# Kernel optimization log

Hardware: AMD Instinct MI355X
Metric: run time of the kernel (lower is better)

The kernel has to match this reference:

```python
import jax, jax.numpy as jnp
import numpy as np

H = 2048
V = 32000
B = 4            # 2 chosen + 2 rejected sequences
T = 1024
BETA = 0.1
IGNORE_INDEX = -100


def setup_inputs() -> dict:
    key = jax.random.key(0)
    k1, k2, k3, k4, k5 = jax.random.split(key, 5)
    x = jax.random.normal(k1, (B, T, H), dtype=jnp.float32)
    ref_x = jax.random.normal(k2, (B, T, H), dtype=jnp.float32)
    y = jax.random.randint(k3, (B, T), 0, V, dtype=jnp.int64)
    # Linear weights scaled ~1/sqrt(H) so logits are well-conditioned
    W = jax.random.normal(k4, (V, H), dtype=jnp.float32) * (1.0 / np.sqrt(H))
    W_ref = jax.random.normal(k5, (V, H), dtype=jnp.float32) * (1.0 / np.sqrt(H))
    return {"x": x, "ref_x": ref_x, "y": y, "W": W, "W_ref": W_ref}


def _avg_seq_logps(h, W, y, mask):
    # h: [B,T,H], W: [V,H] -> average per-sequence log-prob of the target tokens
    logits = jnp.einsum("bth,vh->btv", h, W)                 # [B,T,V]
    logps = jax.nn.log_softmax(logits, axis=-1)
    y_safe = jnp.where(mask, y, 0)
    per_tok = jnp.take_along_axis(logps, y_safe[..., None], axis=-1)[..., 0]  # [B,T]
    m = mask.astype(logps.dtype)
    return (per_tok * m).sum(-1) / m.sum(-1)                  # [B]


def reference(x, ref_x, y, W, W_ref):
    mask = y != IGNORE_INDEX
    logps = _avg_seq_logps(x, W, y, mask)
    # reference model path is computed without gradients (torch.no_grad in Liger)
    ref_logps = jax.lax.stop_gradient(_avg_seq_logps(ref_x, W_ref, y, mask))
    half = B // 2
    chosen, rejected = logps[:half], logps[half:]
    ref_chosen, ref_rejected = ref_logps[:half], ref_logps[half:]
    logits_diff = BETA * ((chosen - ref_chosen) - (rejected - ref_rejected))
    loss = -jax.nn.log_sigmoid(logits_diff).sum() / half
    return loss
```

## Files before the change

kernel.cpp:

```cpp
#include <hip/hip_runtime.h>
#include <cstdint>
#include <cstddef>

#define HDIM 2048
#define VOCAB 32000
#define BT 4096
#define NVB 125
#define BETA_F 0.1f
#define SCALE_X 16.0f
#define SCALE_W 64.0f
#define INV_SC (1.0f / (SCALE_X * SCALE_W))
#define ID_SCALE 0x7f7f7f7f

typedef float f32x16 __attribute__((ext_vector_type(16)));
typedef int i32x4v __attribute__((ext_vector_type(4)));
typedef int i32x8v __attribute__((ext_vector_type(8)));

__device__ __forceinline__ void async_lds16(const void* g, void* l) {
  __builtin_amdgcn_global_load_lds(
      (__attribute__((address_space(1))) void*)g,
      (__attribute__((address_space(3))) void*)l,
      16, 0, 0);
}

#define BAR() __builtin_amdgcn_s_barrier()
#define LGKM0() do { asm volatile("s_waitcnt lgkmcnt(0)" ::: "memory"); \
                     __builtin_amdgcn_sched_barrier(0); } while (0)
#define VMCNT(n) do { asm volatile("s_waitcnt vmcnt(" #n ")" ::: "memory"); \
                      __builtin_amdgcn_sched_barrier(0); } while (0)

__global__ void cast_fp8_kernel(const float* __restrict__ src,
                                uint4* __restrict__ dst, int n16, float scale) {
  int i = blockIdx.x * blockDim.x + threadIdx.x;
  int stride = gridDim.x * blockDim.x;
  for (; i < n16; i += stride) {
    const float4* s = (const float4*)src + (size_t)i * 4;
    uint4 o;
    {
      float4 a = s[0];
      int r = __builtin_amdgcn_cvt_pk_fp8_f32(a.x * scale, a.y * scale, 0, false);
      o.x = __builtin_amdgcn_cvt_pk_fp8_f32(a.z * scale, a.w * scale, r, true);
    }
    {
      float4 a = s[1];
      int r = __builtin_amdgcn_cvt_pk_fp8_f32(a.x * scale, a.y * scale, 0, false);
      o.y = __builtin_amdgcn_cvt_pk_fp8_f32(a.z * scale, a.w * scale, r, true);
    }
    {
      float4 a = s[2];
      int r = __builtin_amdgcn_cvt_pk_fp8_f32(a.x * scale, a.y * scale, 0, false);
      o.z = __builtin_amdgcn_cvt_pk_fp8_f32(a.z * scale, a.w * scale, r, true);
    }
    {
      float4 a = s[3];
      int r = __builtin_amdgcn_cvt_pk_fp8_f32(a.x * scale, a.y * scale, 0, false);
      o.w = __builtin_amdgcn_cvt_pk_fp8_f32(a.z * scale, a.w * scale, r, true);
    }
    dst[i] = o;
  }
}

__global__ __launch_bounds__(512, 2) void gemm_lse256(
    const unsigned char* __restrict__ Xq,
    const unsigned char* __restrict__ Xrq,
    const unsigned char* __restrict__ Wq,
    const unsigned char* __restrict__ Wrq,
    float2* __restrict__ part) {
  __shared__ __align__(16) char lds[2][2][2][8192];

  const int tid = threadIdx.x;
  const int lane = tid & 63;
  const int w = tid >> 6;
  const int wm = w >> 2;
  const int wn = w & 3;
  const int which = blockIdx.y;

  const int lin = blockIdx.x;
  const int nl = (lin & 7) * 250 + (lin >> 3);
  const int mb = nl & 15;
  const int nb = nl >> 4;

  const unsigned char* A = which ? Xrq : Xq;
  const unsigned char* B = which ? Wrq : Wq;
  float2* pp = part + (size_t)which * BT * NVB;

  const int lp = lane ^ (((lane >> 5) & 1) << 1);
  const int srow = (w >> 1) * 32 + (lp & 1) * 16 + ((lp >> 2) & 15);
  const int scol = ((lp >> 1) & 1) * 32 + (w & 1) * 16;
  const unsigned char* Ag = A + (size_t)(mb * 256 + srow) * HDIM + scol;
  const unsigned char* Bg = B + (size_t)(nb * 256 + srow) * HDIM + scol;

#define STAGE(opsel, buf, h, T) do {                                          \
    const unsigned char* _g = (opsel) ? Bg : Ag;                              \
    async_lds16(_g + (size_t)(h) * 128 * HDIM + (T) * 64,                     \
                &lds[buf][opsel][h][0] + w * 1024);                           \
  } while (0)

  const int l31 = lane & 31;
  const int khalf = (lane >> 5) * 32;
#define FRAG32(dst, halfptr, row) do {                                        \
    int _r = (row);                                                           \
    int _p = ((((_r >> 5) << 11) + ((_r & 15) << 6) + khalf +                 \
               (((_r >> 4) & 1) << 4)) ^ (((_r >> 3) & 1) << 5));             \
    i32x4v _lo = *(const i32x4v*)((halfptr) + _p);                            \
    i32x4v _hi = *(const i32x4v*)((halfptr) + _p + 1024);                     \
    dst = (i32x8v){_lo[0], _lo[1], _lo[2], _lo[3],                            \
                   _hi[0], _hi[1], _hi[2], _hi[3]};                           \
  } while (0)

  const char* Ah[2] = { &lds[0][0][wm][0], &lds[1][0][wm][0] };
  const char* Bh[2] = { &lds[0][1][wn >> 1][0], &lds[1][1][wn >> 1][0] };
  const int brow = (wn & 1) * 64;

  f32x16 acc[4][2] = {};
  i32x8v aF0, aF1, bF0, bF1;

#define READ_B(buf) do {                                                      \
    FRAG32(bF0, Bh[buf], brow + l31);                                         \
    FRAG32(bF1, Bh[buf], brow + 32 + l31);                                    \
  } while (0)
#define READ_A2(buf, mi0) do {                                                \
    FRAG32(aF0, Ah[buf], (mi0) * 32 + l31);                                   \
    FRAG32(aF1, Ah[buf], (mi0) * 32 + 32 + l31);                              \
  } while (0)
#define MFMA4(MI0) do {                                                       \
    __builtin_amdgcn_s_setprio(1);                                            \
    acc[MI0][0] = __builtin_amdgcn_mfma_scale_f32_32x32x64_f8f6f4(            \
        aF0, bF0, acc[MI0][0], 0, 0, 0, ID_SCALE, 0, ID_SCALE);               \
    acc[MI0][1] = __builtin_amdgcn_mfma_scale_f32_32x32x64_f8f6f4(            \
        aF0, bF1, acc[MI0][1], 0, 0, 0, ID_SCALE, 0, ID_SCALE);               \
    acc[(MI0) + 1][0] = __builtin_amdgcn_mfma_scale_f32_32x32x64_f8f6f4(      \
        aF1, bF0, acc[(MI0) + 1][0], 0, 0, 0, ID_SCALE, 0, ID_SCALE);         \
    acc[(MI0) + 1][1] = __builtin_amdgcn_mfma_scale_f32_32x32x64_f8f6f4(      \
        aF1, bF1, acc[(MI0) + 1][1], 0, 0, 0, ID_SCALE, 0, ID_SCALE);         \
    __builtin_amdgcn_s_setprio(0);                                            \
  } while (0)

  STAGE(0, 0, 0, 0); STAGE(0, 0, 1, 0); STAGE(1, 0, 0, 0); STAGE(1, 0, 1, 0);
  STAGE(1, 1, 0, 1); STAGE(1, 1, 1, 1);
  VMCNT(2);
  BAR();

  for (int i = 0; i < 16; ++i) {
    const int t1 = 2 * i + 1;
    const int se = (2 * i + 2 > 30) ? 30 : 2 * i + 2;
    const int so = (2 * i + 3 > 31) ? 31 : 2 * i + 3;

    READ_A2(0, 0); READ_B(0);
    STAGE(0, 1, 0, t1); STAGE(0, 1, 1, t1);
    BAR(); LGKM0();
    MFMA4(0);
    BAR();

    READ_A2(0, 2);
    STAGE(1, 0, 0, se); STAGE(1, 0, 1, se);
    VMCNT(2);
    BAR(); LGKM0();
    MFMA4(2);
    BAR();

    READ_A2(1, 0); READ_B(1);
    STAGE(0, 0, 0, se); STAGE(0, 0, 1, se);
    BAR(); LGKM0();
    MFMA4(0);
    BAR();

    READ_A2(1, 2);
    STAGE(1, 1, 0, so); STAGE(1, 1, 1, so);
    VMCNT(2);
    BAR(); LGKM0();
    MFMA4(2);
    BAR();
  }
  VMCNT(0);
  BAR();

  float* red = (float*)&lds[0][0][0][0];
#pragma unroll
  for (int mi = 0; mi < 4; ++mi) {
#pragma unroll
    for (int r = 0; r < 16; ++r) {
      float v0 = acc[mi][0][r] * INV_SC;
      float v1 = acc[mi][1][r] * INV_SC;
      float m = fmaxf(v0, v1);
#pragma unroll
      for (int o = 1; o < 32; o <<= 1) m = fmaxf(m, __shfl_xor(m, o, 64));
      float s = __expf(v0 - m) + __expf(v1 - m);
#pragma unroll
      for (int o = 1; o < 32; o <<= 1) s += __shfl_xor(s, o, 64);
      if (l31 == 0) {
        int row = wm * 128 + mi * 32 + (r & 3) + 8 * (r >> 2) + 4 * (lane >> 5);
        red[wn * 256 + row] = m;
        red[1024 + wn * 256 + row] = s;
      }
    }
  }
  __syncthreads();
  if (tid < 256) {
    float m0 = red[tid], m1 = red[256 + tid], m2 = red[512 + tid], m3 = red[768 + tid];
    float M = fmaxf(fmaxf(m0, m1), fmaxf(m2, m3));
    float S = red[1024 + tid] * __expf(m0 - M) + red[1280 + tid] * __expf(m1 - M) +
              red[1536 + tid] * __expf(m2 - M) + red[1792 + tid] * __expf(m3 - M);
    pp[(size_t)(mb * 256 + tid) * NVB + nb] = make_float2(M, S);
  }
#undef STAGE
#undef FRAG32
#undef READ_B
#undef READ_A2
#undef MFMA4
}

__global__ void target_logit(const float* __restrict__ x, const float* __restrict__ xr,
                             const float* __restrict__ W, const float* __restrict__ Wr,
                             const int* __restrict__ y, float* __restrict__ tlog) {
  int wid = (blockIdx.x * blockDim.x + threadIdx.x) >> 6;
  int lane = threadIdx.x & 63;
  int which = wid >> 12;
  int tok = wid & 4095;
  int yy = y[tok];
  int ys = (yy == -100) ? 0 : yy;
  const float* xv = (which ? xr : x) + (size_t)tok * HDIM;
  const float* wv = (which ? Wr : W) + (size_t)ys * HDIM;
  const float4* x4 = (const float4*)xv;
  const float4* w4 = (const float4*)wv;
  float sum = 0.f;
  for (int i = lane; i < HDIM / 4; i += 64) {
    float4 a = x4[i], b = w4[i];
    sum += a.x * b.x + a.y * b.y + a.z * b.z + a.w * b.w;
  }
#pragma unroll
  for (int o = 1; o < 64; o <<= 1) sum += __shfl_xor(sum, o, 64);
  if (lane == 0) tlog[wid] = sum;
}

__global__ void lse_combine(const float2* __restrict__ part,
                            const float* __restrict__ tlog,
                            float* __restrict__ ptok) {
  int wid = (blockIdx.x * blockDim.x + threadIdx.x) >> 6;
  int lane = threadIdx.x & 63;
  const float2* p = part + (size_t)wid * NVB;
  float m = -INFINITY, s = 0.f;
  for (int i = lane; i < NVB; i += 64) {
    float2 v = p[i];
    float M = fmaxf(m, v.x);
    s = s * __expf(m - M) + v.y * __expf(v.x - M);
    m = M;
  }
#pragma unroll
  for (int o = 1; o < 64; o <<= 1) {
    float mo = __shfl_xor(m, o, 64);
    float so = __shfl_xor(s, o, 64);
    float M = fmaxf(m, mo);
    s = s * __expf(m - M) + so * __expf(mo - M);
    m = M;
  }
  if (lane == 0) ptok[wid] = tlog[wid] - (m + logf(s));
}

__global__ void final_loss(const float* __restrict__ ptok,
                           const int* __restrict__ y, float* __restrict__ out) {
  __shared__ float rs[256];
  __shared__ float rc[256];
  __shared__ float seq[8];
  int tid = threadIdx.x;
  for (int s = 0; s < 8; ++s) {
    int which = s >> 2, b = s & 3;
    float lsum = 0.f, lcnt = 0.f;
    for (int t = tid; t < 1024; t += 256) {
      int yy = y[b * 1024 + t];
      if (yy != -100) {
        lsum += ptok[which * 4096 + b * 1024 + t];
        lcnt += 1.f;
      }
    }
    rs[tid] = lsum; rc[tid] = lcnt;
    __syncthreads();
    for (int o = 128; o > 0; o >>= 1) {
      if (tid < o) { rs[tid] += rs[tid + o]; rc[tid] += rc[tid + o]; }
      __syncthreads();
    }
    if (tid == 0) seq[s] = rs[0] / rc[0];
    __syncthreads();
  }
  if (tid == 0) {
    float d0 = BETA_F * ((seq[0] - seq[4]) - (seq[2] - seq[6]));
    float d1 = BETA_F * ((seq[1] - seq[5]) - (seq[3] - seq[7]));
    auto sp = [](float a) { return fmaxf(a, 0.f) + log1pf(expf(-fabsf(a))); };
    out[0] = (sp(-d0) + sp(-d1)) * 0.5f;
  }
}

extern "C" void kernel_launch(void* const* d_in, const int* in_sizes, int n_in,
                              void* d_out, int out_size, void* d_ws, size_t ws_size,
                              hipStream_t stream) {
  const float* x   = (const float*)d_in[0];
  const float* xr  = (const float*)d_in[1];
  const int*   y   = (const int*)d_in[2];
  const float* Wf  = (const float*)d_in[3];
  const float* Wrf = (const float*)d_in[4];
  float* out = (float*)d_out;

  char* ws = (char*)d_ws;
  size_t off = 0;
  auto alloc = [&](size_t bytes) -> void* {
    void* p = ws + off;
    off = (off + bytes + 255) & ~(size_t)255;
    return p;
  };
  unsigned char* Xq  = (unsigned char*)alloc((size_t)BT * HDIM);
  unsigned char* Xrq = (unsigned char*)alloc((size_t)BT * HDIM);
  unsigned char* Wq  = (unsigned char*)alloc((size_t)VOCAB * HDIM);
  unsigned char* Wrq = (unsigned char*)alloc((size_t)VOCAB * HDIM);
  float2* part = (float2*)alloc((size_t)2 * BT * NVB * sizeof(float2));
  float*  tlog = (float*)alloc((size_t)2 * BT * sizeof(float));
  float*  ptok = (float*)alloc((size_t)2 * BT * sizeof(float));

  cast_fp8_kernel<<<2048, 256, 0, stream>>>(x,  (uint4*)Xq,  BT * HDIM / 16, SCALE_X);
  cast_fp8_kernel<<<2048, 256, 0, stream>>>(xr, (uint4*)Xrq, BT * HDIM / 16, SCALE_X);
  cast_fp8_kernel<<<2048, 256, 0, stream>>>(Wf,  (uint4*)Wq,  VOCAB * HDIM / 16, SCALE_W);
  cast_fp8_kernel<<<2048, 256, 0, stream>>>(Wrf, (uint4*)Wrq, VOCAB * HDIM / 16, SCALE_W);

  dim3 gg(2000, 2);
  gemm_lse256<<<gg, 512, 0, stream>>>(Xq, Xrq, Wq, Wrq, part);

  target_logit<<<2048, 256, 0, stream>>>(x, xr, Wf, Wrf, y, tlog);
  lse_combine<<<2048, 256, 0, stream>>>(part, tlog, ptok);
  final_loss<<<1, 256, 0, stream>>>(ptok, y, out);
}
```

Before: 1.033 ms.

## Use 1024-thread blocks with per-wave 64x64 tiles and interleaved LDS/MFMA schedule

Doubles the GEMM workgroup from 8 to 16 waves, so each wave now owns a 64x64 output tile (four accumulators) instead of 128x64. The main loop is rewritten to interleave individual fragment reads with single MFMAs, prefetching the next stage's fragments before the last MFMA of each K step. It also drops explicit lgkmcnt waits in favor of sched barriers. The aim is better latency hiding and simpler staging (one A and one B async load per thread per stage), at the cost of more LDS traffic per MFMA and one block per CU instead of two.

```diff
diff --git a/kernel.cpp b/kernel.cpp
--- a/kernel.cpp
+++ b/kernel.cpp
@@ -24,8 +24,7 @@
 }
 
 #define BAR() __builtin_amdgcn_s_barrier()
-#define LGKM0() do { asm volatile("s_waitcnt lgkmcnt(0)" ::: "memory"); \
-                     __builtin_amdgcn_sched_barrier(0); } while (0)
+#define SCHED0() __builtin_amdgcn_sched_barrier(0)
 #define VMCNT(n) do { asm volatile("s_waitcnt vmcnt(" #n ")" ::: "memory"); \
                       __builtin_amdgcn_sched_barrier(0); } while (0)
 
@@ -60,7 +59,7 @@
   }
 }
 
-__global__ __launch_bounds__(512, 2) void gemm_lse256(
+__global__ __launch_bounds__(1024) void gemm_lse256(
     const unsigned char* __restrict__ Xq,
     const unsigned char* __restrict__ Xrq,
     const unsigned char* __restrict__ Wq,
@@ -84,16 +83,16 @@
   const unsigned char* B = which ? Wrq : Wq;
   float2* pp = part + (size_t)which * BT * NVB;
 
+  const int wp = w & 7;
   const int lp = lane ^ (((lane >> 5) & 1) << 1);
-  const int srow = (w >> 1) * 32 + (lp & 1) * 16 + ((lp >> 2) & 15);
-  const int scol = ((lp >> 1) & 1) * 32 + (w & 1) * 16;
+  const int srow = (w >> 3) * 128 + (wp >> 1) * 32 + (lp & 1) * 16 + ((lp >> 2) & 15);
+  const int scol = ((lp >> 1) & 1) * 32 + (wp & 1) * 16;
   const unsigned char* Ag = A + (size_t)(mb * 256 + srow) * HDIM + scol;
   const unsigned char* Bg = B + (size_t)(nb * 256 + srow) * HDIM + scol;
 
-#define STAGE(opsel, buf, h, T) do {                                          \
-    const unsigned char* _g = (opsel) ? Bg : Ag;                              \
-    async_lds16(_g + (size_t)(h) * 128 * HDIM + (T) * 64,                     \
-                &lds[buf][opsel][h][0] + w * 1024);                           \
+#define STAGE_AB(buf, T) do {                                                 \
+    async_lds16(Ag + (size_t)(T) * 64, &lds[buf][0][w >> 3][0] + wp * 1024);  \
+    async_lds16(Bg + (size_t)(T) * 64, &lds[buf][1][w >> 3][0] + wp * 1024);  \
   } while (0)
 
   const int l31 = lane & 31;
@@ -108,80 +107,69 @@
                    _hi[0], _hi[1], _hi[2], _hi[3]};                           \
   } while (0)
 
-  const char* Ah[2] = { &lds[0][0][wm][0], &lds[1][0][wm][0] };
+  const char* Ah[2] = { &lds[0][0][wm >> 1][0], &lds[1][0][wm >> 1][0] };
   const char* Bh[2] = { &lds[0][1][wn >> 1][0], &lds[1][1][wn >> 1][0] };
-  const int brow = (wn & 1) * 64;
-
-  f32x16 acc[4][2] = {};
+  const int arow = (wm & 1) * 64 + l31;
+  const int brow = (wn & 1) * 64 + l31;
+
+  f32x16 acc00 = {}, acc01 = {}, acc10 = {}, acc11 = {};
   i32x8v aF0, aF1, bF0, bF1;
 
-#define READ_B(buf) do {                                                      \
-    FRAG32(bF0, Bh[buf], brow + l31);                                         \
-    FRAG32(bF1, Bh[buf], brow + 32 + l31);                                    \
-  } while (0)
-#define READ_A2(buf, mi0) do {                                                \
-    FRAG32(aF0, Ah[buf], (mi0) * 32 + l31);                                   \
-    FRAG32(aF1, Ah[buf], (mi0) * 32 + 32 + l31);                              \
-  } while (0)
-#define MFMA4(MI0) do {                                                       \
+#define MFMA1(ACC, AF, BF) do {                                               \
     __builtin_amdgcn_s_setprio(1);                                            \
-    acc[MI0][0] = __builtin_amdgcn_mfma_scale_f32_32x32x64_f8f6f4(            \
-        aF0, bF0, acc[MI0][0], 0, 0, 0, ID_SCALE, 0, ID_SCALE);               \
-    acc[MI0][1] = __builtin_amdgcn_mfma_scale_f32_32x32x64_f8f6f4(            \
-        aF0, bF1, acc[MI0][1], 0, 0, 0, ID_SCALE, 0, ID_SCALE);               \
-    acc[(MI0) + 1][0] = __builtin_amdgcn_mfma_scale_f32_32x32x64_f8f6f4(      \
-        aF1, bF0, acc[(MI0) + 1][0], 0, 0, 0, ID_SCALE, 0, ID_SCALE);         \
-    acc[(MI0) + 1][1] = __builtin_amdgcn_mfma_scale_f32_32x32x64_f8f6f4(      \
-        aF1, bF1, acc[(MI0) + 1][1], 0, 0, 0, ID_SCALE, 0, ID_SCALE);         \
+    ACC = __builtin_amdgcn_mfma_scale_f32_32x32x64_f8f6f4(                    \
+        AF, BF, ACC, 0, 0, 0, ID_SCALE, 0, ID_SCALE);                         \
     __builtin_amdgcn_s_setprio(0);                                            \
   } while (0)
 
-  STAGE(0, 0, 0, 0); STAGE(0, 0, 1, 0); STAGE(1, 0, 0, 0); STAGE(1, 0, 1, 0);
-  STAGE(1, 1, 0, 1); STAGE(1, 1, 1, 1);
+  STAGE_AB(0, 0);
+  STAGE_AB(1, 1);
   VMCNT(2);
-  BAR();
+  BAR(); SCHED0();
+  FRAG32(aF0, Ah[0], arow);
+  FRAG32(bF0, Bh[0], brow);
+  SCHED0();
 
   for (int i = 0; i < 16; ++i) {
-    const int t1 = 2 * i + 1;
     const int se = (2 * i + 2 > 30) ? 30 : 2 * i + 2;
     const int so = (2 * i + 3 > 31) ? 31 : 2 * i + 3;
 
-    READ_A2(0, 0); READ_B(0);
-    STAGE(0, 1, 0, t1); STAGE(0, 1, 1, t1);
-    BAR(); LGKM0();
-    MFMA4(0);
-    BAR();
-
-    READ_A2(0, 2);
-    STAGE(1, 0, 0, se); STAGE(1, 0, 1, se);
-    VMCNT(2);
-    BAR(); LGKM0();
-    MFMA4(2);
-    BAR();
-
-    READ_A2(1, 0); READ_B(1);
-    STAGE(0, 0, 0, se); STAGE(0, 0, 1, se);
-    BAR(); LGKM0();
-    MFMA4(0);
-    BAR();
-
-    READ_A2(1, 2);
-    STAGE(1, 1, 0, so); STAGE(1, 1, 1, so);
-    VMCNT(2);
-    BAR(); LGKM0();
-    MFMA4(2);
-    BAR();
+    FRAG32(bF1, Bh[0], brow + 32); SCHED0();
+    MFMA1(acc00, aF0, bF0); SCHED0();
+    FRAG32(aF1, Ah[0], arow + 32); SCHED0();
+    MFMA1(acc01, aF0, bF1); SCHED0();
+    MFMA1(acc10, aF1, bF0); SCHED0();
+    VMCNT(0);
+    BAR(); SCHED0();
+    STAGE_AB(0, se);
+    FRAG32(aF0, Ah[1], arow);
+    FRAG32(bF0, Bh[1], brow); SCHED0();
+    MFMA1(acc11, aF1, bF1); SCHED0();
+
+    FRAG32(bF1, Bh[1], brow + 32); SCHED0();
+    MFMA1(acc00, aF0, bF0); SCHED0();
+    FRAG32(aF1, Ah[1], arow + 32); SCHED0();
+    MFMA1(acc01, aF0, bF1); SCHED0();
+    MFMA1(acc10, aF1, bF0); SCHED0();
+    VMCNT(0);
+    BAR(); SCHED0();
+    STAGE_AB(1, so);
+    FRAG32(aF0, Ah[0], arow);
+    FRAG32(bF0, Bh[0], brow); SCHED0();
+    MFMA1(acc11, aF1, bF1); SCHED0();
   }
   VMCNT(0);
-  BAR();
+  BAR(); SCHED0();
 
   float* red = (float*)&lds[0][0][0][0];
 #pragma unroll
-  for (int mi = 0; mi < 4; ++mi) {
+  for (int mi = 0; mi < 2; ++mi) {
+    const f32x16& a0 = mi ? acc10 : acc00;
+    const f32x16& a1 = mi ? acc11 : acc01;
 #pragma unroll
     for (int r = 0; r < 16; ++r) {
-      float v0 = acc[mi][0][r] * INV_SC;
-      float v1 = acc[mi][1][r] * INV_SC;
+      float v0 = a0[r] * INV_SC;
+      float v1 = a1[r] * INV_SC;
       float m = fmaxf(v0, v1);
 #pragma unroll
       for (int o = 1; o < 32; o <<= 1) m = fmaxf(m, __shfl_xor(m, o, 64));
@@ -189,7 +177,7 @@
 #pragma unroll
       for (int o = 1; o < 32; o <<= 1) s += __shfl_xor(s, o, 64);
       if (l31 == 0) {
-        int row = wm * 128 + mi * 32 + (r & 3) + 8 * (r >> 2) + 4 * (lane >> 5);
+        int row = wm * 64 + mi * 32 + (r & 3) + 8 * (r >> 2) + 4 * (lane >> 5);
         red[wn * 256 + row] = m;
         red[1024 + wn * 256 + row] = s;
       }
@@ -203,11 +191,9 @@
               red[1536 + tid] * __expf(m2 - M) + red[1792 + tid] * __expf(m3 - M);
     pp[(size_t)(mb * 256 + tid) * NVB + nb] = make_float2(M, S);
   }
-#undef STAGE
+#undef STAGE_AB
 #undef FRAG32
-#undef READ_B
-#undef READ_A2
-#undef MFMA4
+#undef MFMA1
 }
 
 __global__ void target_logit(const float* __restrict__ x, const float* __restrict__ xr,
@@ -321,7 +307,7 @@
   cast_fp8_kernel<<<2048, 256, 0, stream>>>(Wrf, (uint4*)Wrq, VOCAB * HDIM / 16, SCALE_W);
 
   dim3 gg(2000, 2);
-  gemm_lse256<<<gg, 512, 0, stream>>>(Xq, Xrq, Wq, Wrq, part);
+  gemm_lse256<<<gg, 1024, 0, stream>>>(Xq, Xrq, Wq, Wrq, part);
 
   target_logit<<<2048, 256, 0, stream>>>(x, xr, Wf, Wrf, y, tlog);
   lse_combine<<<2048, 256, 0, stream>>>(part, tlog, ptok);
```

Result: faster. 965.3 us (-6.5%).
